# Kernel tuning notes

Measured on AMD Instinct MI355X. Metric: run time of the kernel, lower is better.

## Reference

```python
import jax, jax.numpy as jnp
import numpy as np

LAMBDA_GEO = 0.5


def setup_inputs() -> dict:
    key = jax.random.key(0)
    embeddings = jax.random.normal(key, (4, 2048, 512), dtype=jnp.float32)
    return {"embeddings": embeddings}


def _geometric_loss(embeddings):
    b, s, d = embeddings.shape
    x = embeddings.reshape(b * s, d)  # [N, d]
    sq_norm = jnp.sum(x * x, axis=-1)  # [N]
    sq = sq_norm[:, None] + sq_norm[None, :] - 2.0 * (x @ x.T)  # [N, N]
    sq = jnp.maximum(sq, 0.0)
    dist = jnp.sqrt(sq)  # torch.cdist(p=2)
    return jnp.mean(jnp.exp(-dist * 0.1)) * 0.1


def reference(embeddings):
    geometric_loss = _geometric_loss(embeddings)
    total_geometric = LAMBDA_GEO * geometric_loss
    return geometric_loss, total_geometric
```

## Files before the change

kernel.cpp:

```cpp
#include <hip/hip_runtime.h>

#define NROWS 8192
#define DIM   512
#define NT    64
#define NTRI  (NT * (NT + 1) / 2)
#define NACC  64

using f32x4 = __attribute__((ext_vector_type(4))) float;

__device__ __forceinline__ unsigned char f2e4m3(float x) {
    unsigned ux = __float_as_uint(x);
    unsigned s  = (ux >> 24) & 0x80u;
    float a = __uint_as_float(ux & 0x7FFFFFFFu);
    a = fminf(a, 448.0f);
    unsigned ua = __float_as_uint(a);
    int eb = (int)(ua >> 23);
    if (eb < 121) eb = 121;
    float step  = __uint_as_float((unsigned)(eb - 3) << 23);
    float istep = __uint_as_float((unsigned)(257 - eb) << 23);
    float q = rintf(a * istep) * step;
    q = fminf(q, 448.0f);
    if (q < 0.001953125f)
        return (unsigned char)s;
    unsigned uq = __float_as_uint(q);
    int eq = (int)(uq >> 23) - 127;
    unsigned byte;
    if (eq < -6) byte = (unsigned)(q * 512.0f);
    else         byte = (unsigned)((eq + 7) << 3) | ((uq >> 20) & 7u);
    return (unsigned char)(s | byte);
}

__global__ __launch_bounds__(256) void norm_convert_kernel(
    const float* __restrict__ X, unsigned char* __restrict__ Xq,
    float* __restrict__ norms, float* __restrict__ acc)
{
    const int tid  = threadIdx.x;
    const int lane = tid & 63;
    const int w    = tid >> 6;
    const int row  = blockIdx.x * 4 + w;

    if (blockIdx.x == 0 && tid < NACC) acc[tid] = 0.0f;

    const float* xr = X + (size_t)row * DIM + lane * 8;
    float4 v0 = *(const float4*)xr;
    float4 v1 = *(const float4*)(xr + 4);

    float s = 0.0f;
    s = fmaf(v0.x, v0.x, s); s = fmaf(v0.y, v0.y, s);
    s = fmaf(v0.z, v0.z, s); s = fmaf(v0.w, v0.w, s);
    s = fmaf(v1.x, v1.x, s); s = fmaf(v1.y, v1.y, s);
    s = fmaf(v1.z, v1.z, s); s = fmaf(v1.w, v1.w, s);

    union { unsigned char b[8]; uint2 v; } pk;
    pk.b[0] = f2e4m3(v0.x); pk.b[1] = f2e4m3(v0.y);
    pk.b[2] = f2e4m3(v0.z); pk.b[3] = f2e4m3(v0.w);
    pk.b[4] = f2e4m3(v1.x); pk.b[5] = f2e4m3(v1.y);
    pk.b[6] = f2e4m3(v1.z); pk.b[7] = f2e4m3(v1.w);

    const int slab = lane >> 3;
    const int cpos = (lane & 7) ^ (row & 7);
    *(uint2*)(Xq + (size_t)row * DIM + slab * 64 + cpos * 8) = pk.v;

    #pragma unroll
    for (int off = 32; off > 0; off >>= 1) s += __shfl_down(s, off, 64);
    if (lane == 0) norms[row] = s;
}

__global__ __launch_bounds__(256, 4) void pair_loss_gemm_kernel(
    const unsigned char* __restrict__ Xq, const float* __restrict__ norms,
    float* __restrict__ acc)
{
    __shared__ __align__(16) char As0[8192];
    __shared__ __align__(16) char As1[8192];
    __shared__ __align__(16) char Bs0[8192];
    __shared__ __align__(16) char Bs1[8192];
    __shared__ float wsum[4];

    int t = blockIdx.x, bi = 0;
    while (t >= (NT - bi)) { t -= (NT - bi); bi++; }
    const int bj = bi + t;

    const int tid  = threadIdx.x;
    const int lane = tid & 63;
    const int w    = tid >> 6;

    const int rowA = bi * 128;
    const int rowB = bj * 128;

    f32x4 accv[4][4];
    const f32x4 zero = {0.0f, 0.0f, 0.0f, 0.0f};
    #pragma unroll
    for (int a = 0; a < 4; a++)
        #pragma unroll
        for (int b = 0; b < 4; b++) accv[a][b] = zero;

    const int r0 = tid >> 1;
    const int h0 = tid & 1;
    const int wb = r0 * 64 + h0 * 32;
    const unsigned char* gA = Xq + (size_t)(rowA + r0) * DIM + h0 * 32;
    const unsigned char* gB = Xq + (size_t)(rowB + r0) * DIM + h0 * 32;

    const int fr  = lane & 15;
    const int q   = lane >> 4;
    const int fo0 = fr * 64 + ((q ^ (fr & 7)) * 8);
    const int wr  = (w & 1) * 64;
    const int wc  = (w >> 1) * 64;

    {
        uint4 pa0 = *(const uint4*)gA;
        uint4 pa1 = *(const uint4*)(gA + 16);
        uint4 pb0 = *(const uint4*)gB;
        uint4 pb1 = *(const uint4*)(gB + 16);
        *(uint4*)(As0 + wb)      = pa0;
        *(uint4*)(As0 + wb + 16) = pa1;
        *(uint4*)(Bs0 + wb)      = pb0;
        *(uint4*)(Bs0 + wb + 16) = pb1;
    }
    __syncthreads();

    char* curA = As0; char* nxtA = As1;
    char* curB = Bs0; char* nxtB = Bs1;

    #pragma unroll 1
    for (int k = 0; k < 8; k++) {
        uint4 pa0, pa1, pb0, pb1;
        const bool more = (k < 7);
        if (more) {
            const int k0 = (k + 1) * 64;
            pa0 = *(const uint4*)(gA + k0);
            pa1 = *(const uint4*)(gA + k0 + 16);
            pb0 = *(const uint4*)(gB + k0);
            pb1 = *(const uint4*)(gB + k0 + 16);
        }

        #pragma unroll
        for (int s = 0; s < 2; s++) {
            const int fo = fo0 ^ (s << 5);
            long af[4], bf[4];
            #pragma unroll
            for (int a = 0; a < 4; a++)
                af[a] = *(const long*)(curA + (wr + a * 16) * 64 + fo);
            #pragma unroll
            for (int b = 0; b < 4; b++)
                bf[b] = *(const long*)(curB + (wc + b * 16) * 64 + fo);
            #pragma unroll
            for (int a = 0; a < 4; a++)
                #pragma unroll
                for (int b = 0; b < 4; b++)
                    accv[a][b] = __builtin_amdgcn_mfma_f32_16x16x32_fp8_fp8(
                        af[a], bf[b], accv[a][b], 0, 0, 0);
        }

        if (more) {
            *(uint4*)(nxtA + wb)      = pa0;
            *(uint4*)(nxtA + wb + 16) = pa1;
            *(uint4*)(nxtB + wb)      = pb0;
            *(uint4*)(nxtB + wb + 16) = pb1;
            __syncthreads();
            char* tA = curA; curA = nxtA; nxtA = tA;
            char* tB = curB; curB = nxtB; nxtB = tB;
        }
    }

    const float wgt = (bi == bj) ? 1.0f : 2.0f;
    float lsum = 0.0f;
    #pragma unroll
    for (int a = 0; a < 4; a++) {
        const int gi0 = rowA + wr + a * 16 + (lane >> 4) * 4;
        #pragma unroll
        for (int b = 0; b < 4; b++) {
            const int gj = rowB + wc + b * 16 + (lane & 15);
            const float nj = norms[gj];
            #pragma unroll
            for (int r = 0; r < 4; r++) {
                const int gi = gi0 + r;
                float sq = fmaf(-2.0f, accv[a][b][r], norms[gi] + nj);
                sq = fmaxf(sq, 0.0f);
                float term = __expf(-0.1f * sqrtf(sq));
                if (gi == gj) term = 1.0f;
                lsum += term;
            }
        }
    }
    lsum *= wgt;
    #pragma unroll
    for (int off = 32; off > 0; off >>= 1) lsum += __shfl_down(lsum, off, 64);
    if (lane == 0) wsum[w] = lsum;
    __syncthreads();
    if (tid == 0)
        atomicAdd(&acc[blockIdx.x & (NACC - 1)],
                  wsum[0] + wsum[1] + wsum[2] + wsum[3]);
}

__global__ void finalize_kernel(const float* __restrict__ acc,
                                float* __restrict__ out)
{
    const int lane = threadIdx.x;
    float s = (lane < NACC) ? acc[lane] : 0.0f;
    #pragma unroll
    for (int off = 32; off > 0; off >>= 1) s += __shfl_down(s, off, 64);
    if (lane == 0) {
        const float inv = 1.0f / ((float)NROWS * (float)NROWS);
        float loss = s * inv * 0.1f;
        out[0] = loss;
        out[1] = 0.5f * loss;
    }
}

extern "C" void kernel_launch(void* const* d_in, const int* in_sizes, int n_in,
                              void* d_out, int out_size, void* d_ws, size_t ws_size,
                              hipStream_t stream)
{
    const float* X = (const float*)d_in[0];
    float* out = (float*)d_out;

    char* ws = (char*)d_ws;
    float*         acc   = (float*)ws;
    float*         norms = (float*)(ws + 1024);
    unsigned char* Xq    = (unsigned char*)(ws + 1024 + 32768);

    norm_convert_kernel<<<NROWS / 4, 256, 0, stream>>>(X, Xq, norms, acc);
    pair_loss_gemm_kernel<<<NTRI, 256, 0, stream>>>(Xq, norms, acc);
    finalize_kernel<<<1, 64, 0, stream>>>(acc, out);
}
```

Baseline: 105.1 us.

## Use 32x32x64 scaled FP8 MFMA with direct global-to-LDS loads

```diff
diff --git a/kernel.cpp b/kernel.cpp
--- a/kernel.cpp
+++ b/kernel.cpp
@@ -6,7 +6,8 @@
 #define NTRI  (NT * (NT + 1) / 2)
 #define NACC  64
 
-using f32x4 = __attribute__((ext_vector_type(4))) float;
+typedef __attribute__((ext_vector_type(16))) float f32x16;
+typedef __attribute__((ext_vector_type(8)))  int   i32x8;
 
 __device__ __forceinline__ unsigned char f2e4m3(float x) {
     unsigned ux = __float_as_uint(x);
@@ -66,6 +67,12 @@
     if (lane == 0) norms[row] = s;
 }
 
+__device__ __forceinline__ void gload16(const void* g, void* l) {
+    __builtin_amdgcn_global_load_lds(
+        (const __attribute__((address_space(1))) unsigned int*)g,
+        (__attribute__((address_space(3))) unsigned int*)l, 16, 0, 0);
+}
+
 __global__ __launch_bounds__(256, 4) void pair_loss_gemm_kernel(
     const unsigned char* __restrict__ Xq, const float* __restrict__ norms,
     float* __restrict__ acc)
@@ -87,35 +94,34 @@
     const int rowA = bi * 128;
     const int rowB = bj * 128;
 
-    f32x4 accv[4][4];
-    const f32x4 zero = {0.0f, 0.0f, 0.0f, 0.0f};
-    #pragma unroll
-    for (int a = 0; a < 4; a++)
-        #pragma unroll
-        for (int b = 0; b < 4; b++) accv[a][b] = zero;
-
-    const int r0 = tid >> 1;
-    const int h0 = tid & 1;
-    const int wb = r0 * 64 + h0 * 32;
-    const unsigned char* gA = Xq + (size_t)(rowA + r0) * DIM + h0 * 32;
-    const unsigned char* gB = Xq + (size_t)(rowB + r0) * DIM + h0 * 32;
-
-    const int fr  = lane & 15;
-    const int q   = lane >> 4;
-    const int fo0 = fr * 64 + ((q ^ (fr & 7)) * 8);
-    const int wr  = (w & 1) * 64;
-    const int wc  = (w >> 1) * 64;
-
-    {
-        uint4 pa0 = *(const uint4*)gA;
-        uint4 pa1 = *(const uint4*)(gA + 16);
-        uint4 pb0 = *(const uint4*)gB;
-        uint4 pb1 = *(const uint4*)(gB + 16);
-        *(uint4*)(As0 + wb)      = pa0;
-        *(uint4*)(As0 + wb + 16) = pa1;
-        *(uint4*)(Bs0 + wb)      = pb0;
-        *(uint4*)(Bs0 + wb + 16) = pb1;
-    }
+    f32x16 accv[2][2];
+    #pragma unroll
+    for (int a = 0; a < 2; a++)
+        #pragma unroll
+        for (int b = 0; b < 2; b++)
+            #pragma unroll
+            for (int r = 0; r < 16; r++) accv[a][b][r] = 0.0f;
+
+    const int rs = w * 32 + (lane >> 2);
+    const int cs = (lane & 3) * 16;
+    const unsigned char* sA0 = Xq + (size_t)(rowA + rs) * DIM + cs;
+    const unsigned char* sA1 = sA0 + (size_t)16 * DIM;
+    const unsigned char* sB0 = Xq + (size_t)(rowB + rs) * DIM + cs;
+    const unsigned char* sB1 = sB0 + (size_t)16 * DIM;
+    const int ldw = w * 2048;
+
+    const int rl = lane & 31;
+    const int qh = lane >> 5;
+    const int sw = lane & 7;
+    const int wr = (w & 1) * 64;
+    const int wc = (w >> 1) * 64;
+    const int raoff = (wr + rl) * 64;
+    const int rboff = (wc + rl) * 64;
+
+    gload16(sA0, As0 + ldw);
+    gload16(sA1, As0 + ldw + 1024);
+    gload16(sB0, Bs0 + ldw);
+    gload16(sB1, Bs0 + ldw + 1024);
     __syncthreads();
 
     char* curA = As0; char* nxtA = As1;
@@ -123,39 +129,35 @@
 
     #pragma unroll 1
     for (int k = 0; k < 8; k++) {
-        uint4 pa0, pa1, pb0, pb1;
         const bool more = (k < 7);
         if (more) {
-            const int k0 = (k + 1) * 64;
-            pa0 = *(const uint4*)(gA + k0);
-            pa1 = *(const uint4*)(gA + k0 + 16);
-            pb0 = *(const uint4*)(gB + k0);
-            pb1 = *(const uint4*)(gB + k0 + 16);
-        }
-
-        #pragma unroll
-        for (int s = 0; s < 2; s++) {
-            const int fo = fo0 ^ (s << 5);
-            long af[4], bf[4];
-            #pragma unroll
-            for (int a = 0; a < 4; a++)
-                af[a] = *(const long*)(curA + (wr + a * 16) * 64 + fo);
-            #pragma unroll
-            for (int b = 0; b < 4; b++)
-                bf[b] = *(const long*)(curB + (wc + b * 16) * 64 + fo);
-            #pragma unroll
-            for (int a = 0; a < 4; a++)
-                #pragma unroll
-                for (int b = 0; b < 4; b++)
-                    accv[a][b] = __builtin_amdgcn_mfma_f32_16x16x32_fp8_fp8(
-                        af[a], bf[b], accv[a][b], 0, 0, 0);
-        }
+            const int ko = (k + 1) * 64;
+            gload16(sA0 + ko, nxtA + ldw);
+            gload16(sA1 + ko, nxtA + ldw + 1024);
+            gload16(sB0 + ko, nxtB + ldw);
+            gload16(sB1 + ko, nxtB + ldw + 1024);
+        }
+
+        union { long l[4]; i32x8 v; } fa0, fa1, fb0, fb1;
+        #pragma unroll
+        for (int i = 0; i < 4; i++) {
+            const int fo = ((4 * qh + i) ^ sw) * 8;
+            fa0.l[i] = *(const long*)(curA + raoff + fo);
+            fa1.l[i] = *(const long*)(curA + raoff + 2048 + fo);
+            fb0.l[i] = *(const long*)(curB + rboff + fo);
+            fb1.l[i] = *(const long*)(curB + rboff + 2048 + fo);
+        }
+
+        accv[0][0] = __builtin_amdgcn_mfma_scale_f32_32x32x64_f8f6f4(
+            fa0.v, fb0.v, accv[0][0], 0, 0, 0, 0x7F7F7F7F, 0, 0x7F7F7F7F);
+        accv[0][1] = __builtin_amdgcn_mfma_scale_f32_32x32x64_f8f6f4(
+            fa0.v, fb1.v, accv[0][1], 0, 0, 0, 0x7F7F7F7F, 0, 0x7F7F7F7F);
+        accv[1][0] = __builtin_amdgcn_mfma_scale_f32_32x32x64_f8f6f4(
+            fa1.v, fb0.v, accv[1][0], 0, 0, 0, 0x7F7F7F7F, 0, 0x7F7F7F7F);
+        accv[1][1] = __builtin_amdgcn_mfma_scale_f32_32x32x64_f8f6f4(
+            fa1.v, fb1.v, accv[1][1], 0, 0, 0, 0x7F7F7F7F, 0, 0x7F7F7F7F);
 
         if (more) {
-            *(uint4*)(nxtA + wb)      = pa0;
-            *(uint4*)(nxtA + wb + 16) = pa1;
-            *(uint4*)(nxtB + wb)      = pb0;
-            *(uint4*)(nxtB + wb + 16) = pb1;
             __syncthreads();
             char* tA = curA; curA = nxtA; nxtA = tA;
             char* tB = curB; curB = nxtB; nxtB = tB;
@@ -163,18 +165,24 @@
     }
 
     const float wgt = (bi == bj) ? 1.0f : 2.0f;
+    const int cl = lane & 31;
+    const int rh = (lane >> 5) * 4;
     float lsum = 0.0f;
     #pragma unroll
-    for (int a = 0; a < 4; a++) {
-        const int gi0 = rowA + wr + a * 16 + (lane >> 4) * 4;
-        #pragma unroll
-        for (int b = 0; b < 4; b++) {
-            const int gj = rowB + wc + b * 16 + (lane & 15);
+    for (int a = 0; a < 2; a++) {
+        const int gia = rowA + wr + a * 32;
+        float ni[16];
+        #pragma unroll
+        for (int r = 0; r < 16; r++)
+            ni[r] = norms[gia + (r & 3) + 8 * (r >> 2) + rh];
+        #pragma unroll
+        for (int b = 0; b < 2; b++) {
+            const int gj = rowB + wc + b * 32 + cl;
             const float nj = norms[gj];
             #pragma unroll
-            for (int r = 0; r < 4; r++) {
-                const int gi = gi0 + r;
-                float sq = fmaf(-2.0f, accv[a][b][r], norms[gi] + nj);
+            for (int r = 0; r < 16; r++) {
+                const int gi = gia + (r & 3) + 8 * (r >> 2) + rh;
+                float sq = fmaf(-2.0f, accv[a][b][r], ni[r] + nj);
                 sq = fmaxf(sq, 0.0f);
                 float term = __expf(-0.1f * sqrtf(sq));
                 if (gi == gj) term = 1.0f;
```

Measured after the change: 106.3 us. No clear change (+1.2%).

## Remap tile order across XCDs and streamline loss epilogue

Applied to the files above, without the earlier changes.

```diff
diff --git a/kernel.cpp b/kernel.cpp
--- a/kernel.cpp
+++ b/kernel.cpp
@@ -66,6 +66,39 @@
     if (lane == 0) norms[row] = s;
 }
 
+template <bool DIAG>
+__device__ __forceinline__ float tile_epilogue(
+    const f32x4 (&accv)[4][4], const float* __restrict__ norms,
+    int rowA, int rowB, int wr, int wc, int lane)
+{
+    const int q4 = (lane >> 4) * 4;
+    const int fr = lane & 15;
+    const float C = -0.14426950408889634f;
+    float njv[4];
+    #pragma unroll
+    for (int b = 0; b < 4; b++) njv[b] = norms[rowB + wc + b * 16 + fr];
+    float lsum = 0.0f;
+    #pragma unroll
+    for (int a = 0; a < 4; a++) {
+        const int gi0 = rowA + wr + a * 16 + q4;
+        const float4 niv = *(const float4*)(norms + gi0);
+        const float ni[4] = {niv.x, niv.y, niv.z, niv.w};
+        #pragma unroll
+        for (int b = 0; b < 4; b++) {
+            const int gj = rowB + wc + b * 16 + fr;
+            #pragma unroll
+            for (int r = 0; r < 4; r++) {
+                float sq = fmaf(-2.0f, accv[a][b][r], ni[r] + njv[b]);
+                sq = fmaxf(sq, 0.0f);
+                float term = exp2f(C * sqrtf(sq));
+                if (DIAG) { if (gi0 + r == gj) term = 1.0f; }
+                lsum += term;
+            }
+        }
+    }
+    return lsum;
+}
+
 __global__ __launch_bounds__(256, 4) void pair_loss_gemm_kernel(
     const unsigned char* __restrict__ Xq, const float* __restrict__ norms,
     float* __restrict__ acc)
@@ -76,7 +109,8 @@
     __shared__ __align__(16) char Bs1[8192];
     __shared__ float wsum[4];
 
-    int t = blockIdx.x, bi = 0;
+    const int bid = (blockIdx.x & 7) * 260 + (blockIdx.x >> 3);
+    int t = bid, bi = 0;
     while (t >= (NT - bi)) { t -= (NT - bi); bi++; }
     const int bj = bi + t;
 
@@ -162,33 +196,16 @@
         }
     }
 
-    const float wgt = (bi == bj) ? 1.0f : 2.0f;
-    float lsum = 0.0f;
-    #pragma unroll
-    for (int a = 0; a < 4; a++) {
-        const int gi0 = rowA + wr + a * 16 + (lane >> 4) * 4;
-        #pragma unroll
-        for (int b = 0; b < 4; b++) {
-            const int gj = rowB + wc + b * 16 + (lane & 15);
-            const float nj = norms[gj];
-            #pragma unroll
-            for (int r = 0; r < 4; r++) {
-                const int gi = gi0 + r;
-                float sq = fmaf(-2.0f, accv[a][b][r], norms[gi] + nj);
-                sq = fmaxf(sq, 0.0f);
-                float term = __expf(-0.1f * sqrtf(sq));
-                if (gi == gj) term = 1.0f;
-                lsum += term;
-            }
-        }
-    }
-    lsum *= wgt;
+    float lsum = (bi == bj)
+        ? tile_epilogue<true >(accv, norms, rowA, rowB, wr, wc, lane)
+        : 2.0f * tile_epilogue<false>(accv, norms, rowA, rowB, wr, wc, lane);
+
     #pragma unroll
     for (int off = 32; off > 0; off >>= 1) lsum += __shfl_down(lsum, off, 64);
     if (lane == 0) wsum[w] = lsum;
     __syncthreads();
     if (tid == 0)
-        atomicAdd(&acc[blockIdx.x & (NACC - 1)],
+        atomicAdd(&acc[bid & (NACC - 1)],
                   wsum[0] + wsum[1] + wsum[2] + wsum[3]);
 }
 
```

Measured after the change: 107.8 us. 2.6% more time.
